# Optimization experiments

Measured on AMD Instinct MI355X. Metric: run time of the kernel, lower is better.

The kernel has to match this reference:

```python
import jax, jax.numpy as jnp
import numpy as np
import math

D_MODEL = 1024
N_HEADS = 16
D_K = D_MODEL // N_HEADS
FFN = 4096
B, S = 4, 1024
EPS = 1e-5


def setup_inputs() -> dict:
    key = jax.random.key(0)
    ks = jax.random.split(key, 24)
    sd = 0.02
    def w(k, shape):
        return jax.random.normal(k, shape, dtype=jnp.float32) * sd
    inp = {
        'x': jax.random.normal(ks[0], (B, S, D_MODEL), dtype=jnp.float32),
        'enc': jax.random.normal(ks[1], (B, S, D_MODEL), dtype=jnp.float32),
        'mask': jnp.tril(jnp.ones((S, S), dtype=jnp.int32)),  # causal look-ahead mask
        # stacked per-head projections [H, d_model, d_k], biases [H, d_k]
        'Wq_self': w(ks[2], (N_HEADS, D_MODEL, D_K)), 'bq_self': w(ks[3], (N_HEADS, D_K)),
        'Wk_self': w(ks[4], (N_HEADS, D_MODEL, D_K)), 'bk_self': w(ks[5], (N_HEADS, D_K)),
        'Wv_self': w(ks[6], (N_HEADS, D_MODEL, D_K)), 'bv_self': w(ks[7], (N_HEADS, D_K)),
        'Wq_x': w(ks[8], (N_HEADS, D_MODEL, D_K)), 'bq_x': w(ks[9], (N_HEADS, D_K)),
        'Wk_x': w(ks[10], (N_HEADS, D_MODEL, D_K)), 'bk_x': w(ks[11], (N_HEADS, D_K)),
        'Wv_x': w(ks[12], (N_HEADS, D_MODEL, D_K)), 'bv_x': w(ks[13], (N_HEADS, D_K)),
        # W_O is SHARED between self- and cross-attention (as in the torch code)
        'Wo': w(ks[14], (D_MODEL, D_MODEL)), 'bo': w(ks[15], (D_MODEL,)),
        'W1': w(ks[16], (D_MODEL, FFN)), 'b1': w(ks[17], (FFN,)),
        'W2': w(ks[18], (FFN, D_MODEL)), 'b2': w(ks[19], (D_MODEL,)),
        'g1': jnp.ones((D_MODEL,), jnp.float32), 'be1': jnp.zeros((D_MODEL,), jnp.float32),
        'g2': jnp.ones((D_MODEL,), jnp.float32), 'be2': jnp.zeros((D_MODEL,), jnp.float32),
        'g3': jnp.ones((D_MODEL,), jnp.float32), 'be3': jnp.zeros((D_MODEL,), jnp.float32),
    }
    return inp


def _layernorm(x, g, b):
    mu = jnp.mean(x, axis=-1, keepdims=True)
    d = x - mu
    var = jnp.mean(d * d, axis=-1, keepdims=True)
    return d * jax.lax.rsqrt(var + EPS) * g + b


def _mha(xq, xkv, Wq, bq, Wk, bk, Wv, bv, mask):
    # batched equivalent of the per-head Python loop
    q = jnp.einsum('bsd,hdk->bhsk', xq, Wq) + bq[None, :, None, :]
    k = jnp.einsum('btd,hdk->bhtk', xkv, Wk) + bk[None, :, None, :]
    v = jnp.einsum('btd,hdk->bhtk', xkv, Wv) + bv[None, :, None, :]
    scores = jnp.einsum('bhsk,bhtk->bhst', q, k) / math.sqrt(D_K)
    if mask is not None:
        scores = jnp.where(mask[None, None] == 0, -jnp.inf, scores)
    attn = jax.nn.softmax(scores, axis=-1)
    z = jnp.einsum('bhst,bhtk->bhsk', attn, v)
    # concat heads along last dim (head i occupies slice i, matching torch.cat)
    b_, h_, s_, k_ = z.shape
    return jnp.transpose(z, (0, 2, 1, 3)).reshape(b_, s_, h_ * k_)


def reference(x, enc, mask, Wq_self, bq_self, Wk_self, bk_self, Wv_self, bv_self,
              Wq_x, bq_x, Wk_x, bk_x, Wv_x, bv_x, Wo, bo, W1, b1, W2, b2,
              g1, be1, g2, be2, g3, be3):
    sa = _mha(x, x, Wq_self, bq_self, Wk_self, bk_self, Wv_self, bv_self, mask)
    x1 = _layernorm(x + sa @ Wo + bo, g1, be1)
    ca = _mha(x1, enc, Wq_x, bq_x, Wk_x, bk_x, Wv_x, bv_x, None)
    x2 = _layernorm(x1 + ca @ Wo + bo, g2, be2)
    ffn = jax.nn.relu(x2 @ W1 + b1) @ W2 + b2
    return _layernorm(x2 + ffn, g3, be3)
```

## Files before the change

kernel.cpp:

```cpp
#include <hip/hip_runtime.h>
#include <cstdint>

typedef __bf16 bf16_t;
typedef bf16_t bf16x8 __attribute__((ext_vector_type(8)));
typedef bf16_t bf16x4 __attribute__((ext_vector_type(4)));
typedef float  f32x4  __attribute__((ext_vector_type(4)));

#define DEVI static __device__ __forceinline__

DEVI void async_ld16(const bf16_t* g, bf16_t* l) {
  __builtin_amdgcn_global_load_lds((const __attribute__((address_space(1))) void*)g,
                                   (__attribute__((address_space(3))) void*)l, 16, 0, 0);
}

struct PrepArgs {
  const float *WqS, *WkS, *WvS, *WqX, *WkX, *WvX, *Wo, *W1, *W2, *x, *enc;
  const float *bqS, *bkS, *bvS, *bkX, *bvX;
  bf16_t *WqkvST, *WqXT, *WkvXT, *WoT, *W1T, *W2T, *xb, *encb;
  float *bqkv, *bkvx;
};

__global__ __launch_bounds__(256)
void k_prep(PrepArgs a)
{
  __shared__ float tile[32][33];
  const int blk = blockIdx.x, tid = threadIdx.x;
  const int tx = tid & 31, ty = tid >> 5;

  const float* src = nullptr;
  bf16_t* dst = nullptr;
  int srcLd = 0, dstLd = 0, m0 = 0, n0 = 0;
  bool do_tr = false;

  if (blk < 6144) {
    int j = blk >> 10, q = blk & 1023;
    src = j == 0 ? a.WqS : j == 1 ? a.WkS : j == 2 ? a.WvS : j == 3 ? a.WqX : j == 4 ? a.WkX : a.WvX;
    dst = j == 0 ? a.WqkvST : j == 1 ? a.WqkvST + 1048576 : j == 2 ? a.WqkvST + 2097152
        : j == 3 ? a.WqXT : j == 4 ? a.WkvXT : a.WkvXT + 1048576;
    int batch = q >> 6, rem = q & 63;
    src += (long)batch * 65536; dst += (long)batch * 65536;
    srcLd = 64; dstLd = 1024;
    n0 = (rem & 1) * 32; m0 = (rem >> 1) * 32;
    do_tr = true;
  } else if (blk < 7168) {
    int q = blk - 6144;
    src = a.Wo; dst = a.WoT; srcLd = 1024; dstLd = 1024;
    m0 = (q >> 5) * 32; n0 = (q & 31) * 32; do_tr = true;
  } else if (blk < 11264) {
    int q = blk - 7168;
    src = a.W1; dst = a.W1T; srcLd = 4096; dstLd = 1024;
    m0 = (q >> 7) * 32; n0 = (q & 127) * 32; do_tr = true;
  } else if (blk < 15360) {
    int q = blk - 11264;
    src = a.W2; dst = a.W2T; srcLd = 1024; dstLd = 4096;
    m0 = (q >> 5) * 32; n0 = (q & 31) * 32; do_tr = true;
  } else if (blk < 16384) {
    long base = (long)(blk - 15360) * 4096 + tid * 4;
#pragma unroll
    for (int u = 0; u < 4; u++) {
      float4 v = *(const float4*)(a.x + base + u * 1024);
      bf16x4 o; o[0] = (bf16_t)v.x; o[1] = (bf16_t)v.y; o[2] = (bf16_t)v.z; o[3] = (bf16_t)v.w;
      *(bf16x4*)(a.xb + base + u * 1024) = o;
    }
    return;
  } else if (blk < 17408) {
    long base = (long)(blk - 16384) * 4096 + tid * 4;
#pragma unroll
    for (int u = 0; u < 4; u++) {
      float4 v = *(const float4*)(a.enc + base + u * 1024);
      bf16x4 o; o[0] = (bf16_t)v.x; o[1] = (bf16_t)v.y; o[2] = (bf16_t)v.z; o[3] = (bf16_t)v.w;
      *(bf16x4*)(a.encb + base + u * 1024) = o;
    }
    return;
  } else {
    int gi = (blk - 17408) * 1024 + tid * 4;
#pragma unroll
    for (int j = 0; j < 4; j++) {
      int i = gi + j;
      if (i < 1024)      a.bqkv[i] = a.bqS[i];
      else if (i < 2048) a.bqkv[i] = a.bkS[i - 1024];
      else if (i < 3072) a.bqkv[i] = a.bvS[i - 2048];
      else if (i < 4096) a.bkvx[i - 3072] = a.bkX[i - 3072];
      else if (i < 5120) a.bkvx[i - 3072] = a.bvX[i - 4096];
    }
    return;
  }

  if (do_tr) {
#pragma unroll
    for (int i = 0; i < 4; i++)
      tile[ty + i * 8][tx] = src[(long)(m0 + ty + i * 8) * srcLd + n0 + tx];
    __syncthreads();
#pragma unroll
    for (int i = 0; i < 4; i++)
      dst[(long)(n0 + ty + i * 8) * dstLd + m0 + tx] = (bf16_t)tile[tx][ty + i * 8];
  }
}

template<int OUT_MODE, int RELU, int VOFF>
__global__ __launch_bounds__(256, 2)
void k_gemm(const bf16_t* __restrict__ A, int lda,
            const bf16_t* __restrict__ Bt, int ldb,
            const float* __restrict__ bias,
            bf16_t* __restrict__ C, int ldc,
            bf16_t* __restrict__ Vt,
            bf16_t* __restrict__ p0, bf16_t* __restrict__ p1,
            bf16_t* __restrict__ p2, bf16_t* __restrict__ p3,
            int Ktot, int nx)
{
  __shared__ bf16_t As[2][128 * 32];
  __shared__ bf16_t Bs[2][128 * 32];
  const int tid  = threadIdx.x;
  const int wave = tid >> 6, lane = tid & 63;
  const int quad = lane >> 4, m16 = lane & 15;

  int lin = blockIdx.x;
  int perx = gridDim.x >> 3;
  int t = (lin & 7) * perx + (lin >> 3);
  const int bcol = (t % nx) * 128, brow = (t / nx) * 128;
  const int wr = (wave >> 1) * 64, wc = (wave & 1) * 64;

  const int Kper = Ktot / gridDim.z;
  const int k0 = blockIdx.z * Kper;

  f32x4 acc[4][4];
#pragma unroll
  for (int i = 0; i < 4; i++)
#pragma unroll
    for (int j = 0; j < 4; j++) acc[i][j] = (f32x4){0.f, 0.f, 0.f, 0.f};

  auto stage = [&](int kt, int buf) {
#pragma unroll
    for (int i = 0; i < 2; i++) {
      int rg = wave * 2 + i;
      async_ld16(A  + (long)(brow + rg * 16 + m16) * lda + kt + quad * 8, As[buf] + rg * 512);
      async_ld16(Bt + (long)(bcol + rg * 16 + m16) * ldb + kt + quad * 8, Bs[buf] + rg * 512);
    }
  };

  stage(k0, 0);
  __syncthreads();

  const int nIter = Kper >> 5;
  for (int it = 0; it < nIter; it++) {
    const int cur = it & 1;
    if (it + 1 < nIter) stage(k0 + (it + 1) * 32, cur ^ 1);

    bf16x8 af[4], bfr[4];
#pragma unroll
    for (int tt = 0; tt < 4; tt++) {
      af[tt]  = *(const bf16x8*)(As[cur] + ((wr + tt * 16) >> 4) * 512 + quad * 128 + m16 * 8);
      bfr[tt] = *(const bf16x8*)(Bs[cur] + ((wc + tt * 16) >> 4) * 512 + quad * 128 + m16 * 8);
    }
#pragma unroll
    for (int i = 0; i < 4; i++)
#pragma unroll
      for (int j = 0; j < 4; j++)
        acc[i][j] = __builtin_amdgcn_mfma_f32_16x16x32_bf16(af[i], bfr[j], acc[i][j], 0, 0, 0);

    __syncthreads();
  }

  if (OUT_MODE == 1) {
    bf16_t* P = blockIdx.z == 0 ? p0 : blockIdx.z == 1 ? p1 : blockIdx.z == 2 ? p2 : p3;
#pragma unroll
    for (int i = 0; i < 4; i++)
#pragma unroll
      for (int j = 0; j < 4; j++) {
        int col = bcol + wc + j * 16 + m16;
#pragma unroll
        for (int r = 0; r < 4; r++) {
          int row = brow + wr + i * 16 + quad * 4 + r;
          P[(long)row * ldc + col] = (bf16_t)acc[i][j][r];
        }
      }
  } else {
#pragma unroll
    for (int i = 0; i < 4; i++)
#pragma unroll
      for (int j = 0; j < 4; j++) {
        int col = bcol + wc + j * 16 + m16;
        float bv = bias[col];
        if (VOFF && col >= VOFF) {
          int hh = (col - VOFF) >> 6, dd = col & 63;
          int row0 = brow + wr + i * 16 + quad * 4;
          int bb = row0 >> 10, seq = row0 & 1023;
          bf16x4 pk;
#pragma unroll
          for (int r = 0; r < 4; r++) pk[r] = (bf16_t)(acc[i][j][r] + bv);
          *(bf16x4*)(Vt + (long)(bb * 16 + hh) * 65536 + dd * 1024 + seq) = pk;
        } else {
#pragma unroll
          for (int r = 0; r < 4; r++) {
            int row = brow + wr + i * 16 + quad * 4 + r;
            float v = acc[i][j][r] + bv;
            if (RELU) v = v > 0.f ? v : 0.f;
            C[(long)row * ldc + col] = (bf16_t)v;
          }
        }
      }
  }
}

template<int LN, int RESID, int OUTF, int OUTB>
__global__ __launch_bounds__(256)
void k_reduce4(const bf16_t* __restrict__ p0, const bf16_t* __restrict__ p1,
               const bf16_t* __restrict__ p2, const bf16_t* __restrict__ p3,
               const float* __restrict__ bias, const float* __restrict__ resid,
               const float* __restrict__ gamma, const float* __restrict__ beta,
               float* __restrict__ outf, bf16_t* __restrict__ outb)
{
  constexpr int D = 1024;
  __shared__ float red[8];
  int row = blockIdx.x, tid = threadIdx.x;
  long off = (long)row * D + tid * 4;
  bf16x4 a0 = *(const bf16x4*)(p0 + off);
  bf16x4 a1 = *(const bf16x4*)(p1 + off);
  bf16x4 a2 = *(const bf16x4*)(p2 + off);
  bf16x4 a3 = *(const bf16x4*)(p3 + off);
  float4 bb4 = *(const float4*)(bias + tid * 4);
  float4 v;
  v.x = (float)a0[0] + (float)a1[0] + (float)a2[0] + (float)a3[0] + bb4.x;
  v.y = (float)a0[1] + (float)a1[1] + (float)a2[1] + (float)a3[1] + bb4.y;
  v.z = (float)a0[2] + (float)a1[2] + (float)a2[2] + (float)a3[2] + bb4.z;
  v.w = (float)a0[3] + (float)a1[3] + (float)a2[3] + (float)a3[3] + bb4.w;
  if (RESID) {
    float4 q = *(const float4*)(resid + off);
    v.x += q.x; v.y += q.y; v.z += q.z; v.w += q.w;
  }
  float4 y = v;
  if (LN) {
    float s  = v.x + v.y + v.z + v.w;
    float sq = v.x * v.x + v.y * v.y + v.z * v.z + v.w * v.w;
#pragma unroll
    for (int o = 1; o < 64; o <<= 1) {
      s  += __shfl_xor(s, o, 64);
      sq += __shfl_xor(sq, o, 64);
    }
    int wave = tid >> 6, lane = tid & 63;
    if (lane == 0) { red[wave * 2] = s; red[wave * 2 + 1] = sq; }
    __syncthreads();
    float ts = red[0] + red[2] + red[4] + red[6];
    float tq = red[1] + red[3] + red[5] + red[7];
    float mu = ts * (1.f / D);
    float var = tq * (1.f / D) - mu * mu;
    float rstd = rsqrtf(var + 1e-5f);
    float4 g  = *(const float4*)(gamma + tid * 4);
    float4 be = *(const float4*)(beta + tid * 4);
    y.x = (v.x - mu) * rstd * g.x + be.x;
    y.y = (v.y - mu) * rstd * g.y + be.y;
    y.z = (v.z - mu) * rstd * g.z + be.z;
    y.w = (v.w - mu) * rstd * g.w + be.w;
  }
  if (OUTF) *(float4*)(outf + off) = y;
  if (OUTB) {
    bf16x4 o;
    o[0] = (bf16_t)y.x; o[1] = (bf16_t)y.y; o[2] = (bf16_t)y.z; o[3] = (bf16_t)y.w;
    *(bf16x4*)(outb + off) = o;
  }
}

template<int CAUSAL>
__global__ __launch_bounds__(256, 2)
void k_attn(const bf16_t* __restrict__ Q, int ldq,
            const bf16_t* __restrict__ Kp, int ldk,
            const bf16_t* __restrict__ Vt,
            bf16_t* __restrict__ O)
{
  constexpr int S = 1024;
  __shared__ bf16_t Kls[4096];
  __shared__ bf16_t Vls[4096];
  __shared__ bf16_t Pls[4][32 * 72];

  const int tid = threadIdx.x;
  const int wave = tid >> 6, lane = tid & 63;
  const int quad = lane >> 4, m16 = lane & 15;
  const int qt = blockIdx.x, bh = blockIdx.y, b = bh >> 4, h = bh & 15;
  const int qbase = qt * 128 + wave * 32;

  bf16x8 qf[2][2];
#pragma unroll
  for (int rh = 0; rh < 2; rh++) {
    const bf16_t* qp = Q + (long)(b * S + qbase + rh * 16 + m16) * ldq + h * 64 + quad * 8;
    qf[rh][0] = *(const bf16x8*)qp;
    qf[rh][1] = *(const bf16x8*)(qp + 32);
  }

  f32x4 o_acc[2][4];
#pragma unroll
  for (int rh = 0; rh < 2; rh++)
#pragma unroll
    for (int t = 0; t < 4; t++) o_acc[rh][t] = (f32x4){0.f, 0.f, 0.f, 0.f};
  float rsum[2][4];
#pragma unroll
  for (int rh = 0; rh < 2; rh++)
#pragma unroll
    for (int r = 0; r < 4; r++) rsum[rh][r] = 0.f;

  const int nch = CAUSAL ? (2 * qt + 2) : 16;
  for (int c = 0; c < nch; c++) {
    __syncthreads();
#pragma unroll
    for (int i = 0; i < 2; i++) {
      int t2 = wave * 2 + i;
      int rg = t2 & 3, ph = t2 >> 2;
      async_ld16(Kp + (long)(b * S + c * 64 + rg * 16 + m16) * ldk + h * 64 + ph * 32 + quad * 8,
                 Kls + t2 * 512);
      async_ld16(Vt + (long)bh * 65536 + (rg * 16 + m16) * 1024 + c * 64 + ph * 32 + quad * 8,
                 Vls + t2 * 512);
    }
    __syncthreads();

    f32x4 s[2][4];
#pragma unroll
    for (int t = 0; t < 4; t++) {
      bf16x8 k0 = *(const bf16x8*)(Kls + (0 * 4 + t) * 512 + quad * 128 + m16 * 8);
      bf16x8 k1 = *(const bf16x8*)(Kls + (1 * 4 + t) * 512 + quad * 128 + m16 * 8);
#pragma unroll
      for (int rh = 0; rh < 2; rh++) {
        f32x4 z = (rh == 0 || true) ? (f32x4){0.f, 0.f, 0.f, 0.f} : (f32x4){0.f, 0.f, 0.f, 0.f};
        z = __builtin_amdgcn_mfma_f32_16x16x32_bf16(qf[rh][0], k0, z, 0, 0, 0);
        z = __builtin_amdgcn_mfma_f32_16x16x32_bf16(qf[rh][1], k1, z, 0, 0, 0);
        s[rh][t] = z;
      }
    }

    bf16_t* pw = Pls[wave];
#pragma unroll
    for (int rh = 0; rh < 2; rh++)
#pragma unroll
      for (int r = 0; r < 4; r++) {
        int qg = qbase + rh * 16 + quad * 4 + r;
#pragma unroll
        for (int t = 0; t < 4; t++) {
          float v = s[rh][t][r] * 0.125f;
          float p;
          if (CAUSAL) {
            int kvg = c * 64 + t * 16 + m16;
            p = (kvg <= qg) ? __expf(v) : 0.f;
          } else {
            p = __expf(v);
          }
          rsum[rh][r] += p;
          pw[(rh * 16 + quad * 4 + r) * 72 + t * 16 + m16] = (bf16_t)p;
        }
      }

    bf16x8 pf[2][2];
#pragma unroll
    for (int rh = 0; rh < 2; rh++)
#pragma unroll
      for (int kvh = 0; kvh < 2; kvh++)
        pf[rh][kvh] = *(const bf16x8*)(pw + (rh * 16 + m16) * 72 + kvh * 32 + quad * 8);
#pragma unroll
    for (int t = 0; t < 4; t++) {
      bf16x8 v0 = *(const bf16x8*)(Vls + (0 * 4 + t) * 512 + quad * 128 + m16 * 8);
      bf16x8 v1 = *(const bf16x8*)(Vls + (1 * 4 + t) * 512 + quad * 128 + m16 * 8);
#pragma unroll
      for (int rh = 0; rh < 2; rh++) {
        o_acc[rh][t] = __builtin_amdgcn_mfma_f32_16x16x32_bf16(pf[rh][0], v0, o_acc[rh][t], 0, 0, 0);
        o_acc[rh][t] = __builtin_amdgcn_mfma_f32_16x16x32_bf16(pf[rh][1], v1, o_acc[rh][t], 0, 0, 0);
      }
    }
  }

#pragma unroll
  for (int rh = 0; rh < 2; rh++)
#pragma unroll
    for (int r = 0; r < 4; r++) {
      float v = rsum[rh][r];
      v += __shfl_xor(v, 1, 64);
      v += __shfl_xor(v, 2, 64);
      v += __shfl_xor(v, 4, 64);
      v += __shfl_xor(v, 8, 64);
      rsum[rh][r] = 1.f / v;
    }
#pragma unroll
  for (int rh = 0; rh < 2; rh++)
#pragma unroll
    for (int t = 0; t < 4; t++)
#pragma unroll
      for (int r = 0; r < 4; r++) {
        int row = b * S + qbase + rh * 16 + quad * 4 + r;
        int col = h * 64 + t * 16 + m16;
        O[(long)row * 1024 + col] = (bf16_t)(o_acc[rh][t][r] * rsum[rh][r]);
      }
}

extern "C" void kernel_launch(void* const* d_in, const int* in_sizes, int n_in,
                              void* d_out, int out_size, void* d_ws, size_t ws_size,
                              hipStream_t stream)
{
  const float* x   = (const float*)d_in[0];
  const float* enc = (const float*)d_in[1];
  const float* WqS = (const float*)d_in[3];
  const float* bqS = (const float*)d_in[4];
  const float* WkS = (const float*)d_in[5];
  const float* bkS = (const float*)d_in[6];
  const float* WvS = (const float*)d_in[7];
  const float* bvS = (const float*)d_in[8];
  const float* WqX = (const float*)d_in[9];
  const float* bqX = (const float*)d_in[10];
  const float* WkX = (const float*)d_in[11];
  const float* bkX = (const float*)d_in[12];
  const float* WvX = (const float*)d_in[13];
  const float* bvX = (const float*)d_in[14];
  const float* Wo  = (const float*)d_in[15];
  const float* bo  = (const float*)d_in[16];
  const float* W1  = (const float*)d_in[17];
  const float* b1  = (const float*)d_in[18];
  const float* W2  = (const float*)d_in[19];
  const float* b2  = (const float*)d_in[20];
  const float* g1  = (const float*)d_in[21];
  const float* be1 = (const float*)d_in[22];
  const float* g2  = (const float*)d_in[23];
  const float* be2 = (const float*)d_in[24];
  const float* g3  = (const float*)d_in[25];
  const float* be3 = (const float*)d_in[26];

  char* ws = (char*)d_ws;
  const long MBy = 1048576;
  bf16_t* WqkvST = (bf16_t*)(ws + 0 * MBy);
  bf16_t* WqXT   = (bf16_t*)(ws + 6 * MBy);
  bf16_t* WkvXT  = (bf16_t*)(ws + 8 * MBy);
  bf16_t* WoT    = (bf16_t*)(ws + 12 * MBy);
  bf16_t* W1T    = (bf16_t*)(ws + 14 * MBy);
  bf16_t* W2T    = (bf16_t*)(ws + 22 * MBy);
  float*  bqkvS  = (float*)(ws + 30 * MBy);
  float*  bkvX   = (float*)(ws + 30 * MBy + 16384);
  bf16_t* xb     = (bf16_t*)(ws + 31 * MBy);
  bf16_t* Qx     = xb;
  bf16_t* encb   = (bf16_t*)(ws + 39 * MBy);
  float*  x1f    = (float*)(ws + 47 * MBy);
  bf16_t* x1b    = (bf16_t*)(ws + 63 * MBy);
  bf16_t* Z      = (bf16_t*)(ws + 71 * MBy);
  bf16_t* QK     = (bf16_t*)(ws + 79 * MBy);
  bf16_t* Kenc   = (bf16_t*)(ws + 79 * MBy);
  bf16_t* Vt     = (bf16_t*)(ws + 95 * MBy);
  bf16_t* pa0 = (bf16_t*)(ws + 95 * MBy);
  bf16_t* pa1 = (bf16_t*)(ws + 103 * MBy);
  bf16_t* pa2 = (bf16_t*)(ws + 111 * MBy);
  bf16_t* pa3 = (bf16_t*)(ws + 119 * MBy);
  bf16_t* Hbuf = (bf16_t*)(ws + 95 * MBy);
  bf16_t* pf0 = (bf16_t*)(ws + 0 * MBy);
  bf16_t* pf1 = (bf16_t*)(ws + 8 * MBy);
  bf16_t* pf2 = (bf16_t*)(ws + 31 * MBy);
  bf16_t* pf3 = (bf16_t*)(ws + 39 * MBy);

  dim3 tb(256);

  PrepArgs pa;
  pa.WqS = WqS; pa.WkS = WkS; pa.WvS = WvS; pa.WqX = WqX; pa.WkX = WkX; pa.WvX = WvX;
  pa.Wo = Wo; pa.W1 = W1; pa.W2 = W2; pa.x = x; pa.enc = enc;
  pa.bqS = bqS; pa.bkS = bkS; pa.bvS = bvS; pa.bkX = bkX; pa.bvX = bvX;
  pa.WqkvST = WqkvST; pa.WqXT = WqXT; pa.WkvXT = WkvXT; pa.WoT = WoT;
  pa.W1T = W1T; pa.W2T = W2T; pa.xb = xb; pa.encb = encb;
  pa.bqkv = bqkvS; pa.bkvx = bkvX;
  k_prep<<<dim3(17413), tb, 0, stream>>>(pa);

  k_gemm<0, 0, 2048><<<dim3(768, 1, 1), tb, 0, stream>>>(
      xb, 1024, WqkvST, 1024, bqkvS, QK, 2048, Vt,
      nullptr, nullptr, nullptr, nullptr, 1024, 24);
  k_attn<1><<<dim3(8, 64), tb, 0, stream>>>(QK, 2048, QK + 1024, 2048, Vt, Z);
  k_gemm<1, 0, 0><<<dim3(256, 1, 4), tb, 0, stream>>>(
      Z, 1024, WoT, 1024, nullptr, nullptr, 1024, nullptr,
      pa0, pa1, pa2, pa3, 1024, 8);
  k_reduce4<1, 1, 1, 1><<<dim3(4096), tb, 0, stream>>>(
      pa0, pa1, pa2, pa3, bo, x, g1, be1, x1f, x1b);

  k_gemm<1, 0, 0><<<dim3(256, 1, 4), tb, 0, stream>>>(
      x1b, 1024, WqXT, 1024, nullptr, nullptr, 1024, nullptr,
      pa0, pa1, pa2, pa3, 1024, 8);
  k_reduce4<0, 0, 0, 1><<<dim3(4096), tb, 0, stream>>>(
      pa0, pa1, pa2, pa3, bqX, nullptr, nullptr, nullptr, nullptr, Qx);
  k_gemm<0, 0, 1024><<<dim3(512, 1, 1), tb, 0, stream>>>(
      encb, 1024, WkvXT, 1024, bkvX, Kenc, 1024, Vt,
      nullptr, nullptr, nullptr, nullptr, 1024, 16);
  k_attn<0><<<dim3(8, 64), tb, 0, stream>>>(Qx, 1024, Kenc, 1024, Vt, Z);
  k_gemm<1, 0, 0><<<dim3(256, 1, 4), tb, 0, stream>>>(
      Z, 1024, WoT, 1024, nullptr, nullptr, 1024, nullptr,
      pa0, pa1, pa2, pa3, 1024, 8);
  k_reduce4<1, 1, 1, 1><<<dim3(4096), tb, 0, stream>>>(
      pa0, pa1, pa2, pa3, bo, x1f, g2, be2, x1f, x1b);

  k_gemm<0, 1, 0><<<dim3(1024, 1, 1), tb, 0, stream>>>(
      x1b, 1024, W1T, 1024, b1, Hbuf, 4096, nullptr,
      nullptr, nullptr, nullptr, nullptr, 1024, 32);
  k_gemm<1, 0, 0><<<dim3(256, 1, 4), tb, 0, stream>>>(
      Hbuf, 4096, W2T, 4096, nullptr, nullptr, 1024, nullptr,
      pf0, pf1, pf2, pf3, 4096, 8);
  k_reduce4<1, 1, 1, 0><<<dim3(4096), tb, 0, stream>>>(
      pf0, pf1, pf2, pf3, b2, x1f, g3, be3, (float*)d_out, nullptr);
}
```

Baseline: 597.8 us.

## Merge self and cross KV projection GEMMs, double-buffer attention K/V, prescale Q

Puts the self-attention QKV projection and the encoder K/V projection into one 1280-block launch, so the encoder projection runs alongside the first GEMM and gets its own K and V^T buffers. The workspace layout is reshuffled so both V^T buffers stay alive. The attention kernel now double-buffers K/V tiles in LDS, prefetching the next chunk while computing the current one. The 1/sqrt(d_k) scale is folded into Q when Q is written, removing a multiply per score. The cost is a larger LDS footprint per attention block and more complex buffer aliasing.

```diff
diff --git a/kernel.cpp b/kernel.cpp
--- a/kernel.cpp
+++ b/kernel.cpp
@@ -97,13 +97,12 @@
   }
 }
 
-template<int OUT_MODE, int RELU, int VOFF>
+template<int OUT_MODE, int RELU>
 __global__ __launch_bounds__(256, 2)
 void k_gemm(const bf16_t* __restrict__ A, int lda,
             const bf16_t* __restrict__ Bt, int ldb,
             const float* __restrict__ bias,
             bf16_t* __restrict__ C, int ldc,
-            bf16_t* __restrict__ Vt,
             bf16_t* __restrict__ p0, bf16_t* __restrict__ p1,
             bf16_t* __restrict__ p2, bf16_t* __restrict__ p3,
             int Ktot, int nx)
@@ -181,28 +180,108 @@
       for (int j = 0; j < 4; j++) {
         int col = bcol + wc + j * 16 + m16;
         float bv = bias[col];
-        if (VOFF && col >= VOFF) {
-          int hh = (col - VOFF) >> 6, dd = col & 63;
-          int row0 = brow + wr + i * 16 + quad * 4;
-          int bb = row0 >> 10, seq = row0 & 1023;
-          bf16x4 pk;
-#pragma unroll
-          for (int r = 0; r < 4; r++) pk[r] = (bf16_t)(acc[i][j][r] + bv);
-          *(bf16x4*)(Vt + (long)(bb * 16 + hh) * 65536 + dd * 1024 + seq) = pk;
-        } else {
-#pragma unroll
-          for (int r = 0; r < 4; r++) {
-            int row = brow + wr + i * 16 + quad * 4 + r;
-            float v = acc[i][j][r] + bv;
-            if (RELU) v = v > 0.f ? v : 0.f;
-            C[(long)row * ldc + col] = (bf16_t)v;
-          }
+#pragma unroll
+        for (int r = 0; r < 4; r++) {
+          int row = brow + wr + i * 16 + quad * 4 + r;
+          float v = acc[i][j][r] + bv;
+          if (RELU) v = v > 0.f ? v : 0.f;
+          C[(long)row * ldc + col] = (bf16_t)v;
         }
       }
   }
 }
 
-template<int LN, int RESID, int OUTF, int OUTB>
+__global__ __launch_bounds__(256, 2)
+void k_gemm_qkv(const bf16_t* __restrict__ A0, const bf16_t* __restrict__ B0,
+                const float* __restrict__ bias0, bf16_t* __restrict__ C0, bf16_t* __restrict__ Vt0,
+                const bf16_t* __restrict__ A1, const bf16_t* __restrict__ B1,
+                const float* __restrict__ bias1, bf16_t* __restrict__ C1, bf16_t* __restrict__ Vt1)
+{
+  __shared__ bf16_t As[2][128 * 32];
+  __shared__ bf16_t Bs[2][128 * 32];
+  const int tid  = threadIdx.x;
+  const int wave = tid >> 6, lane = tid & 63;
+  const int quad = lane >> 4, m16 = lane & 15;
+
+  int lin = blockIdx.x;
+  int perx = gridDim.x >> 3;
+  int t = (lin & 7) * perx + (lin >> 3);
+
+  const bf16_t *A, *Bt; const float* bias; bf16_t *C, *Vt;
+  int nx, ldc, voff, qthresh, tl;
+  if (t < 768) {
+    A = A0; Bt = B0; bias = bias0; C = C0; Vt = Vt0;
+    nx = 24; ldc = 2048; voff = 2048; qthresh = 1024; tl = t;
+  } else {
+    A = A1; Bt = B1; bias = bias1; C = C1; Vt = Vt1;
+    nx = 16; ldc = 1024; voff = 1024; qthresh = 0; tl = t - 768;
+  }
+  const int bcol = (tl % nx) * 128, brow = (tl / nx) * 128;
+  const int wr = (wave >> 1) * 64, wc = (wave & 1) * 64;
+
+  f32x4 acc[4][4];
+#pragma unroll
+  for (int i = 0; i < 4; i++)
+#pragma unroll
+    for (int j = 0; j < 4; j++) acc[i][j] = (f32x4){0.f, 0.f, 0.f, 0.f};
+
+  auto stage = [&](int kt, int buf) {
+#pragma unroll
+    for (int i = 0; i < 2; i++) {
+      int rg = wave * 2 + i;
+      async_ld16(A  + (long)(brow + rg * 16 + m16) * 1024 + kt + quad * 8, As[buf] + rg * 512);
+      async_ld16(Bt + (long)(bcol + rg * 16 + m16) * 1024 + kt + quad * 8, Bs[buf] + rg * 512);
+    }
+  };
+
+  stage(0, 0);
+  __syncthreads();
+
+  for (int it = 0; it < 32; it++) {
+    const int cur = it & 1;
+    if (it + 1 < 32) stage((it + 1) * 32, cur ^ 1);
+
+    bf16x8 af[4], bfr[4];
+#pragma unroll
+    for (int tt = 0; tt < 4; tt++) {
+      af[tt]  = *(const bf16x8*)(As[cur] + ((wr + tt * 16) >> 4) * 512 + quad * 128 + m16 * 8);
+      bfr[tt] = *(const bf16x8*)(Bs[cur] + ((wc + tt * 16) >> 4) * 512 + quad * 128 + m16 * 8);
+    }
+#pragma unroll
+    for (int i = 0; i < 4; i++)
+#pragma unroll
+      for (int j = 0; j < 4; j++)
+        acc[i][j] = __builtin_amdgcn_mfma_f32_16x16x32_bf16(af[i], bfr[j], acc[i][j], 0, 0, 0);
+
+    __syncthreads();
+  }
+
+#pragma unroll
+  for (int i = 0; i < 4; i++)
+#pragma unroll
+    for (int j = 0; j < 4; j++) {
+      int col = bcol + wc + j * 16 + m16;
+      float bv = bias[col];
+      if (col >= voff) {
+        int hh = (col - voff) >> 6, dd = col & 63;
+        int row0 = brow + wr + i * 16 + quad * 4;
+        int bb = row0 >> 10, seq = row0 & 1023;
+        bf16x4 pk;
+#pragma unroll
+        for (int r = 0; r < 4; r++) pk[r] = (bf16_t)(acc[i][j][r] + bv);
+        *(bf16x4*)(Vt + (long)(bb * 16 + hh) * 65536 + dd * 1024 + seq) = pk;
+      } else {
+        float sc = (col < qthresh) ? 0.125f : 1.0f;
+#pragma unroll
+        for (int r = 0; r < 4; r++) {
+          int row = brow + wr + i * 16 + quad * 4 + r;
+          C[(long)row * ldc + col] = (bf16_t)((acc[i][j][r] + bv) * sc);
+        }
+      }
+    }
+}
+
+template<int LN, int RESID, int OUTF, int OUTB, int QS>
 __global__ __launch_bounds__(256)
 void k_reduce4(const bf16_t* __restrict__ p0, const bf16_t* __restrict__ p1,
                const bf16_t* __restrict__ p2, const bf16_t* __restrict__ p3,
@@ -254,6 +333,7 @@
   }
   if (OUTF) *(float4*)(outf + off) = y;
   if (OUTB) {
+    if (QS) { y.x *= 0.125f; y.y *= 0.125f; y.z *= 0.125f; y.w *= 0.125f; }
     bf16x4 o;
     o[0] = (bf16_t)y.x; o[1] = (bf16_t)y.y; o[2] = (bf16_t)y.z; o[3] = (bf16_t)y.w;
     *(bf16x4*)(outb + off) = o;
@@ -268,8 +348,8 @@
             bf16_t* __restrict__ O)
 {
   constexpr int S = 1024;
-  __shared__ bf16_t Kls[4096];
-  __shared__ bf16_t Vls[4096];
+  __shared__ bf16_t Kls[2][4096];
+  __shared__ bf16_t Vls[2][4096];
   __shared__ bf16_t Pls[4][32 * 72];
 
   const int tid = threadIdx.x;
@@ -297,28 +377,34 @@
 #pragma unroll
     for (int r = 0; r < 4; r++) rsum[rh][r] = 0.f;
 
-  const int nch = CAUSAL ? (2 * qt + 2) : 16;
-  for (int c = 0; c < nch; c++) {
-    __syncthreads();
+  auto stage = [&](int c, int buf) {
 #pragma unroll
     for (int i = 0; i < 2; i++) {
       int t2 = wave * 2 + i;
       int rg = t2 & 3, ph = t2 >> 2;
       async_ld16(Kp + (long)(b * S + c * 64 + rg * 16 + m16) * ldk + h * 64 + ph * 32 + quad * 8,
-                 Kls + t2 * 512);
+                 Kls[buf] + t2 * 512);
       async_ld16(Vt + (long)bh * 65536 + (rg * 16 + m16) * 1024 + c * 64 + ph * 32 + quad * 8,
-                 Vls + t2 * 512);
-    }
+                 Vls[buf] + t2 * 512);
+    }
+  };
+
+  const int nch = CAUSAL ? (2 * qt + 2) : 16;
+  stage(0, 0);
+
+  for (int c = 0; c < nch; c++) {
     __syncthreads();
+    const int cur = c & 1;
+    if (c + 1 < nch) stage(c + 1, cur ^ 1);
 
     f32x4 s[2][4];
 #pragma unroll
     for (int t = 0; t < 4; t++) {
-      bf16x8 k0 = *(const bf16x8*)(Kls + (0 * 4 + t) * 512 + quad * 128 + m16 * 8);
-      bf16x8 k1 = *(const bf16x8*)(Kls + (1 * 4 + t) * 512 + quad * 128 + m16 * 8);
+      bf16x8 k0 = *(const bf16x8*)(Kls[cur] + (0 * 4 + t) * 512 + quad * 128 + m16 * 8);
+      bf16x8 k1 = *(const bf16x8*)(Kls[cur] + (1 * 4 + t) * 512 + quad * 128 + m16 * 8);
 #pragma unroll
       for (int rh = 0; rh < 2; rh++) {
-        f32x4 z = (rh == 0 || true) ? (f32x4){0.f, 0.f, 0.f, 0.f} : (f32x4){0.f, 0.f, 0.f, 0.f};
+        f32x4 z = (f32x4){0.f, 0.f, 0.f, 0.f};
         z = __builtin_amdgcn_mfma_f32_16x16x32_bf16(qf[rh][0], k0, z, 0, 0, 0);
         z = __builtin_amdgcn_mfma_f32_16x16x32_bf16(qf[rh][1], k1, z, 0, 0, 0);
         s[rh][t] = z;
@@ -333,7 +419,7 @@
         int qg = qbase + rh * 16 + quad * 4 + r;
 #pragma unroll
         for (int t = 0; t < 4; t++) {
-          float v = s[rh][t][r] * 0.125f;
+          float v = s[rh][t][r];
           float p;
           if (CAUSAL) {
             int kvg = c * 64 + t * 16 + m16;
@@ -354,8 +440,8 @@
         pf[rh][kvh] = *(const bf16x8*)(pw + (rh * 16 + m16) * 72 + kvh * 32 + quad * 8);
 #pragma unroll
     for (int t = 0; t < 4; t++) {
-      bf16x8 v0 = *(const bf16x8*)(Vls + (0 * 4 + t) * 512 + quad * 128 + m16 * 8);
-      bf16x8 v1 = *(const bf16x8*)(Vls + (1 * 4 + t) * 512 + quad * 128 + m16 * 8);
+      bf16x8 v0 = *(const bf16x8*)(Vls[cur] + (0 * 4 + t) * 512 + quad * 128 + m16 * 8);
+      bf16x8 v1 = *(const bf16x8*)(Vls[cur] + (1 * 4 + t) * 512 + quad * 128 + m16 * 8);
 #pragma unroll
       for (int rh = 0; rh < 2; rh++) {
         o_acc[rh][t] = __builtin_amdgcn_mfma_f32_16x16x32_bf16(pf[rh][0], v0, o_acc[rh][t], 0, 0, 0);
@@ -435,17 +521,18 @@
   bf16_t* x1b    = (bf16_t*)(ws + 63 * MBy);
   bf16_t* Z      = (bf16_t*)(ws + 71 * MBy);
   bf16_t* QK     = (bf16_t*)(ws + 79 * MBy);
-  bf16_t* Kenc   = (bf16_t*)(ws + 79 * MBy);
-  bf16_t* Vt     = (bf16_t*)(ws + 95 * MBy);
-  bf16_t* pa0 = (bf16_t*)(ws + 95 * MBy);
-  bf16_t* pa1 = (bf16_t*)(ws + 103 * MBy);
-  bf16_t* pa2 = (bf16_t*)(ws + 111 * MBy);
+  bf16_t* Kenc   = (bf16_t*)(ws + 95 * MBy);
+  bf16_t* VtS    = (bf16_t*)(ws + 103 * MBy);
+  bf16_t* VtX    = (bf16_t*)(ws + 111 * MBy);
+  bf16_t* pa0 = (bf16_t*)(ws + 79 * MBy);
+  bf16_t* pa1 = (bf16_t*)(ws + 87 * MBy);
+  bf16_t* pa2 = (bf16_t*)(ws + 103 * MBy);
   bf16_t* pa3 = (bf16_t*)(ws + 119 * MBy);
-  bf16_t* Hbuf = (bf16_t*)(ws + 95 * MBy);
+  bf16_t* Hbuf = (bf16_t*)(ws + 79 * MBy);
   bf16_t* pf0 = (bf16_t*)(ws + 0 * MBy);
-  bf16_t* pf1 = (bf16_t*)(ws + 8 * MBy);
-  bf16_t* pf2 = (bf16_t*)(ws + 31 * MBy);
-  bf16_t* pf3 = (bf16_t*)(ws + 39 * MBy);
+  bf16_t* pf1 = (bf16_t*)(ws + 31 * MBy);
+  bf16_t* pf2 = (bf16_t*)(ws + 39 * MBy);
+  bf16_t* pf3 = (bf16_t*)(ws + 63 * MBy);
 
   dim3 tb(256);
 
@@ -458,37 +545,30 @@
   pa.bqkv = bqkvS; pa.bkvx = bkvX;
   k_prep<<<dim3(17413), tb, 0, stream>>>(pa);
 
-  k_gemm<0, 0, 2048><<<dim3(768, 1, 1), tb, 0, stream>>>(
-      xb, 1024, WqkvST, 1024, bqkvS, QK, 2048, Vt,
-      nullptr, nullptr, nullptr, nullptr, 1024, 24);
-  k_attn<1><<<dim3(8, 64), tb, 0, stream>>>(QK, 2048, QK + 1024, 2048, Vt, Z);
-  k_gemm<1, 0, 0><<<dim3(256, 1, 4), tb, 0, stream>>>(
-      Z, 1024, WoT, 1024, nullptr, nullptr, 1024, nullptr,
-      pa0, pa1, pa2, pa3, 1024, 8);
-  k_reduce4<1, 1, 1, 1><<<dim3(4096), tb, 0, stream>>>(
+  k_gemm_qkv<<<dim3(1280), tb, 0, stream>>>(
+      xb, WqkvST, bqkvS, QK, VtS,
+      encb, WkvXT, bkvX, Kenc, VtX);
+
+  k_attn<1><<<dim3(8, 64), tb, 0, stream>>>(QK, 2048, QK + 1024, 2048, VtS, Z);
+  k_gemm<1, 0><<<dim3(256, 1, 4), tb, 0, stream>>>(
+      Z, 1024, WoT, 1024, nullptr, nullptr, 1024, pa0, pa1, pa2, pa3, 1024, 8);
+  k_reduce4<1, 1, 1, 1, 0><<<dim3(4096), tb, 0, stream>>>(
       pa0, pa1, pa2, pa3, bo, x, g1, be1, x1f, x1b);
 
-  k_gemm<1, 0, 0><<<dim3(256, 1, 4), tb, 0, stream>>>(
-      x1b, 1024, WqXT, 1024, nullptr, nullptr, 1024, nullptr,
-      pa0, pa1, pa2, pa3, 1024, 8);
-  k_reduce4<0, 0, 0, 1><<<dim3(4096), tb, 0, stream>>>(
+  k_gemm<1, 0><<<dim3(256, 1, 4), tb, 0, stream>>>(
+      x1b, 1024, WqXT, 1024, nullptr, nullptr, 1024, pa0, pa1, pa2, pa3, 1024, 8);
+  k_reduce4<0, 0, 0, 1, 1><<<dim3(4096), tb, 0, stream>>>(
       pa0, pa1, pa2, pa3, bqX, nullptr, nullptr, nullptr, nullptr, Qx);
-  k_gemm<0, 0, 1024><<<dim3(512, 1, 1), tb, 0, stream>>>(
-      encb, 1024, WkvXT, 1024, bkvX, Kenc, 1024, Vt,
-      nullptr, nullptr, nullptr, nullptr, 1024, 16);
-  k_attn<0><<<dim3(8, 64), tb, 0, stream>>>(Qx, 1024, Kenc, 1024, Vt, Z);
-  k_gemm<1, 0, 0><<<dim3(256, 1, 4), tb, 0, stream>>>(
-      Z, 1024, WoT, 1024, nullptr, nullptr, 1024, nullptr,
-      pa0, pa1, pa2, pa3, 1024, 8);
-  k_reduce4<1, 1, 1, 1><<<dim3(4096), tb, 0, stream>>>(
+  k_attn<0><<<dim3(8, 64), tb, 0, stream>>>(Qx, 1024, Kenc, 1024, VtX, Z);
+  k_gemm<1, 0><<<dim3(256, 1, 4), tb, 0, stream>>>(
+      Z, 1024, WoT, 1024, nullptr, nullptr, 1024, pa0, pa1, pa2, pa3, 1024, 8);
+  k_reduce4<1, 1, 1, 1, 0><<<dim3(4096), tb, 0, stream>>>(
       pa0, pa1, pa2, pa3, bo, x1f, g2, be2, x1f, x1b);
 
-  k_gemm<0, 1, 0><<<dim3(1024, 1, 1), tb, 0, stream>>>(
-      x1b, 1024, W1T, 1024, b1, Hbuf, 4096, nullptr,
-      nullptr, nullptr, nullptr, nullptr, 1024, 32);
-  k_gemm<1, 0, 0><<<dim3(256, 1, 4), tb, 0, stream>>>(
-      Hbuf, 4096, W2T, 4096, nullptr, nullptr, 1024, nullptr,
-      pf0, pf1, pf2, pf3, 4096, 8);
-  k_reduce4<1, 1, 1, 0><<<dim3(4096), tb, 0, stream>>>(
+  k_gemm<0, 1><<<dim3(1024), tb, 0, stream>>>(
+      x1b, 1024, W1T, 1024, b1, Hbuf, 4096, nullptr, nullptr, nullptr, nullptr, 1024, 32);
+  k_gemm<1, 0><<<dim3(256, 1, 4), tb, 0, stream>>>(
+      Hbuf, 4096, W2T, 4096, nullptr, nullptr, 1024, pf0, pf1, pf2, pf3, 4096, 8);
+  k_reduce4<1, 1, 1, 0, 0><<<dim3(4096), tb, 0, stream>>>(
       pf0, pf1, pf2, pf3, b2, x1f, g3, be3, (float*)d_out, nullptr);
 }
```

After: 603.8 us. No clear change (+1.0%).
